# Kernel tuning notes

Hardware: AMD Instinct MI355X
Metric: run time of the kernel (lower is better)

The kernel has to match this reference:

```python
import jax, jax.numpy as jnp
import numpy as np
from jax import lax

EPOCHS = 10  # self.epoch in the torch module


def setup_inputs() -> dict:
    key = jax.random.key(0)
    k1, k2 = jax.random.split(key)
    # (num_patches, groups, channels_per_group, kh, kw)
    patches = jax.random.normal(k1, (40000, 4, 16, 5, 5), dtype=jnp.float32)
    # torch: torch.randn([groups, K, D]) * 0.1
    centroids_init = jax.random.normal(k2, (4, 64, 400), dtype=jnp.float32) * 0.1
    return {"patches": patches, "centroids_init": centroids_init}


def reference(patches, centroids_init):
    N, G, C, H, W = patches.shape
    K = centroids_init.shape[1]
    D = C * H * W
    # [G, N, D] flattened patches per group
    pf = jnp.transpose(patches.reshape(N, G, D), (1, 0, 2))

    def step(centroids, _):
        # half squared norm of each centroid: [G, K]
        c2 = 0.5 * jnp.sum(centroids * centroids, axis=2)
        # scores[g,n,k] = <c_gk, p_gn> - 0.5||c_gk||^2  (max over k == nearest centroid)
        scores = jnp.einsum('gkd,gnd->gnk', centroids, pf) - c2[:, None, :]
        labels = jnp.argmax(scores, axis=2)                       # [G, N]
        S = jax.nn.one_hot(labels, K, dtype=pf.dtype)             # [G, N, K]
        summation = jnp.einsum('gnk,gnd->gkd', S, pf)             # [G, K, D]
        counts = jnp.sum(S, axis=1)                               # [G, K]
        new_c = summation / jnp.where(counts == 0, 1.0, counts)[:, :, None]
        # torch: centroids[:, where(counts==0)[1], :] = 0  -> zero that cluster
        # index across ALL groups if empty in any group
        bad = jnp.any(counts == 0, axis=0)                        # [K]
        new_c = jnp.where(bad[None, :, None], 0.0, new_c)
        return new_c, None

    centroids, _ = lax.scan(step, centroids_init, None, length=EPOCHS)
    # reshape to conv weight layout (out_channels, channels_per_group, kh, kw)
    return centroids.reshape(G * K, C, H, W)
```

## Files before the change

kernel.cpp:

```cpp
#include <hip/hip_runtime.h>

#define NPTS   40000
#define NG     4
#define NK     64
#define ND     400
#define PT     256
#define NCHUNK 25
#define NTILES 157
#define NSPL   16

typedef _Float16 f16x4 __attribute__((ext_vector_type(4)));
typedef float    f32x4 __attribute__((ext_vector_type(4)));

__global__ __launch_bounds__(256)
void assign_kernel(const float* __restrict__ patches,
                   const float* __restrict__ cent,
                   int*   __restrict__ lr,
                   int*   __restrict__ pcnt)
{
    const int g    = blockIdx.y;
    const int tile = blockIdx.x;
    const int t    = threadIdx.x;
    const int n0   = tile * PT;

    __shared__ _Float16 A1[PT][20];
    __shared__ _Float16 A2[PT][20];
    __shared__ _Float16 B1[NK][20];
    __shared__ _Float16 B2[NK][20];
    __shared__ float c2p[NK][4];
    __shared__ float c2s[NK];
    __shared__ int   cnt[NK];

    if (t < NK) cnt[t] = 0;

    {
        int k = t >> 2, j = t & 3;
        const float* c = cent + ((size_t)g * NK + k) * ND + 100 * j;
        float s = 0.0f;
        #pragma unroll
        for (int d = 0; d < 100; d += 4) {
            float4 v = *(const float4*)(c + d);
            s = fmaf(v.x, v.x, fmaf(v.y, v.y, fmaf(v.z, v.z, fmaf(v.w, v.w, s))));
        }
        c2p[k][j] = s;
    }
    __syncthreads();
    if (t < NK) c2s[t] = 2048.0f * (c2p[t][0] + c2p[t][1] + c2p[t][2] + c2p[t][3]);

    const int w   = t >> 6;
    const int l   = t & 63;
    const int q   = l >> 4;
    const int r15 = l & 15;

    int nn = n0 + t; if (nn >= NPTS) nn = NPTS - 1;
    const float* prow = patches + ((size_t)nn * NG + g) * ND;
    const float* crow = cent + ((size_t)g * NK + (t >> 2)) * ND + 4 * (t & 3);

    f32x4 acc[4][4];
    {
        f32x4 z = {0.f, 0.f, 0.f, 0.f};
        #pragma unroll
        for (int i = 0; i < 4; ++i)
            #pragma unroll
            for (int j = 0; j < 4; ++j) acc[i][j] = z;
    }

    float4 pp[4]; float4 pc;
    #pragma unroll
    for (int j = 0; j < 4; ++j) pp[j] = *(const float4*)(prow + 4 * j);
    pc = *(const float4*)(crow);

    for (int c = 0; c < NCHUNK; ++c) {
        #pragma unroll
        for (int j = 0; j < 4; ++j) {
            float4 v = pp[j];
            float s0 = v.x * 64.0f, s1 = v.y * 64.0f, s2 = v.z * 64.0f, s3 = v.w * 64.0f;
            _Float16 a0 = (_Float16)s0, a1 = (_Float16)s1, a2 = (_Float16)s2, a3 = (_Float16)s3;
            f16x4 h1 = {a0, a1, a2, a3};
            f16x4 h2 = {(_Float16)(s0 - (float)a0), (_Float16)(s1 - (float)a1),
                        (_Float16)(s2 - (float)a2), (_Float16)(s3 - (float)a3)};
            *(f16x4*)&A1[t][4 * j] = h1;
            *(f16x4*)&A2[t][4 * j] = h2;
        }
        {
            float4 v = pc;
            float s0 = v.x * 64.0f, s1 = v.y * 64.0f, s2 = v.z * 64.0f, s3 = v.w * 64.0f;
            _Float16 a0 = (_Float16)s0, a1 = (_Float16)s1, a2 = (_Float16)s2, a3 = (_Float16)s3;
            f16x4 h1 = {a0, a1, a2, a3};
            f16x4 h2 = {(_Float16)(s0 - (float)a0), (_Float16)(s1 - (float)a1),
                        (_Float16)(s2 - (float)a2), (_Float16)(s3 - (float)a3)};
            int cc = t >> 2, jj = t & 3;
            *(f16x4*)&B1[cc][4 * jj] = h1;
            *(f16x4*)&B2[cc][4 * jj] = h2;
        }
        __syncthreads();

        if (c + 1 < NCHUNK) {
            const int d0 = (c + 1) * 16;
            #pragma unroll
            for (int j = 0; j < 4; ++j) pp[j] = *(const float4*)(prow + d0 + 4 * j);
            pc = *(const float4*)(crow + d0);
        }

        f16x4 a1v[4], a2v[4], b1v[4], b2v[4];
        #pragma unroll
        for (int pi = 0; pi < 4; ++pi) {
            int p = 64 * w + 16 * pi + r15;
            a1v[pi] = *(const f16x4*)&A1[p][4 * q];
            a2v[pi] = *(const f16x4*)&A2[p][4 * q];
        }
        #pragma unroll
        for (int cj = 0; cj < 4; ++cj) {
            int n = 16 * cj + r15;
            b1v[cj] = *(const f16x4*)&B1[n][4 * q];
            b2v[cj] = *(const f16x4*)&B2[n][4 * q];
        }
        #pragma unroll
        for (int pi = 0; pi < 4; ++pi)
            #pragma unroll
            for (int cj = 0; cj < 4; ++cj) {
                acc[pi][cj] = __builtin_amdgcn_mfma_f32_16x16x16f16(a2v[pi], b1v[cj], acc[pi][cj], 0, 0, 0);
                acc[pi][cj] = __builtin_amdgcn_mfma_f32_16x16x16f16(a1v[pi], b2v[cj], acc[pi][cj], 0, 0, 0);
                acc[pi][cj] = __builtin_amdgcn_mfma_f32_16x16x16f16(a1v[pi], b1v[cj], acc[pi][cj], 0, 0, 0);
            }
        __syncthreads();
    }

    #pragma unroll
    for (int pi = 0; pi < 4; ++pi) {
        #pragma unroll
        for (int r = 0; r < 4; ++r) {
            float m  = acc[pi][0][r] - c2s[r15];
            int best = r15;
            #pragma unroll
            for (int cj = 1; cj < 4; ++cj) {
                int n = 16 * cj + r15;
                float s = acc[pi][cj][r] - c2s[n];
                if (s > m) { m = s; best = n; }
            }
            #pragma unroll
            for (int off = 1; off < 16; off <<= 1) {
                float om = __shfl_xor(m, off);
                int   ob = __shfl_xor(best, off);
                if (om > m || (om == m && ob < best)) { m = om; best = ob; }
            }
            if (r15 == 0) {
                int p  = 64 * w + 16 * pi + 4 * q + r;
                int np = n0 + p;
                if (np < NPTS) {
                    int rk = atomicAdd(&cnt[best], 1);
                    lr[(size_t)g * NPTS + np] = (rk << 8) | best;
                }
            }
        }
    }
    __syncthreads();
    if (t < NK) pcnt[((size_t)g * NTILES + tile) * NK + t] = cnt[t];
}

__global__ __launch_bounds__(256)
void scan_kernel(const int* __restrict__ pcnt,
                 int* __restrict__ tilebase,
                 int* __restrict__ cbase,
                 int* __restrict__ counts)
{
    const int g = blockIdx.x;
    const int t = threadIdx.x;
    __shared__ int cnt_tk[NTILES * NK];
    __shared__ int totals[NK];
    __shared__ int kbase[NK];

    for (int i = t; i < NTILES * NK; i += 256)
        cnt_tk[i] = pcnt[(size_t)g * NTILES * NK + i];
    __syncthreads();

    if (t < NK) {
        int s = 0;
        for (int tl = 0; tl < NTILES; ++tl) s += cnt_tk[tl * NK + t];
        totals[t] = s;
    }
    __syncthreads();
    if (t == 0) {
        int run = 0;
        for (int k = 0; k < NK; ++k) { kbase[k] = run; run += totals[k]; }
    }
    __syncthreads();
    if (t < NK) {
        counts[g * NK + t] = totals[t];
        cbase[g * NK + t]  = kbase[t];
        int run = kbase[t];
        for (int tl = 0; tl < NTILES; ++tl) {
            tilebase[((size_t)g * NTILES + tl) * NK + t] = run;
            run += cnt_tk[tl * NK + t];
        }
    }
}

__global__ __launch_bounds__(256)
void scatter_kernel(const int* __restrict__ lr,
                    const int* __restrict__ tilebase,
                    int* __restrict__ order)
{
    const int tile = blockIdx.x, g = blockIdx.y, t = threadIdx.x;
    const int n = tile * PT + t;
    if (n < NPTS) {
        int packed = lr[(size_t)g * NPTS + n];
        int L = packed & 63, r = packed >> 8;
        order[(size_t)g * NPTS + tilebase[((size_t)g * NTILES + tile) * NK + L] + r] = n;
    }
}

__global__ __launch_bounds__(512, 2)
void gather_kernel(const float* __restrict__ patches,
                   const int*   __restrict__ order,
                   const int*   __restrict__ cbase,
                   const int*   __restrict__ counts,
                   float* __restrict__ psum)
{
    const int s = blockIdx.x, k = blockIdx.y, g = blockIdx.z;
    const int t = threadIdx.x;
    const int base = cbase[g * NK + k];
    const int cnt  = counts[g * NK + k];
    const int start = base + (cnt * s) / NSPL;
    const int end   = base + (cnt * (s + 1)) / NSPL;

    const int slot = t / 100;
    const int q    = t - slot * 100;

    float4 acc = make_float4(0.f, 0.f, 0.f, 0.f);
    if (t < 500) {
        const int* ord = order + (size_t)g * NPTS;
        #pragma unroll 4
        for (int i = start + slot; i < end; i += 5) {
            int n = ord[i];
            float4 v = *(const float4*)(patches + ((size_t)n * NG + g) * ND + 4 * q);
            acc.x += v.x; acc.y += v.y; acc.z += v.z; acc.w += v.w;
        }
    }

    __shared__ float sums[ND];
    for (int i = t; i < ND; i += 512) sums[i] = 0.0f;
    __syncthreads();
    if (t < 500) {
        atomicAdd(&sums[4 * q + 0], acc.x);
        atomicAdd(&sums[4 * q + 1], acc.y);
        atomicAdd(&sums[4 * q + 2], acc.z);
        atomicAdd(&sums[4 * q + 3], acc.w);
    }
    __syncthreads();
    if (t < 100) {
        float* dst = psum + (((size_t)(g * NK + k)) * NSPL + s) * ND + 4 * t;
        *(float4*)dst = *(const float4*)&sums[4 * t];
    }
}

__global__ __launch_bounds__(128)
void update_kernel(const float* __restrict__ psum,
                   const int*   __restrict__ counts,
                   float* __restrict__ outc)
{
    const int gk = blockIdx.x;
    const int g = gk >> 6, k = gk & 63;
    const int t = threadIdx.x;

    const bool bad = (counts[0 * NK + k] == 0) | (counts[1 * NK + k] == 0) |
                     (counts[2 * NK + k] == 0) | (counts[3 * NK + k] == 0);
    const int  c  = counts[g * NK + k];
    const float inv = 1.0f / (float)(c == 0 ? 1 : c);

    if (t < 100) {
        float4 s = make_float4(0.f, 0.f, 0.f, 0.f);
        const float* p = psum + ((size_t)gk * NSPL) * ND + 4 * t;
        #pragma unroll
        for (int sp = 0; sp < NSPL; ++sp) {
            float4 v = *(const float4*)(p + (size_t)sp * ND);
            s.x += v.x; s.y += v.y; s.z += v.z; s.w += v.w;
        }
        float4 o;
        o.x = bad ? 0.0f : s.x * inv;
        o.y = bad ? 0.0f : s.y * inv;
        o.z = bad ? 0.0f : s.z * inv;
        o.w = bad ? 0.0f : s.w * inv;
        *(float4*)(outc + (size_t)gk * ND + 4 * t) = o;
    }
}

extern "C" void kernel_launch(void* const* d_in, const int* in_sizes, int n_in,
                              void* d_out, int out_size, void* d_ws, size_t ws_size,
                              hipStream_t stream)
{
    const float* patches = (const float*)d_in[0];
    const float* cinit   = (const float*)d_in[1];
    float* out = (float*)d_out;

    const size_t CSZ = (size_t)NG * NK * ND;
    float* centA = (float*)d_ws;
    float* centB = centA + CSZ;
    int* lr       = (int*)(centB + CSZ);
    int* pcnt     = lr + (size_t)NG * NPTS;
    int* tilebase = pcnt + (size_t)NG * NTILES * NK;
    int* cbase    = tilebase + (size_t)NG * NTILES * NK;
    int* counts   = cbase + NG * NK;
    int* order    = counts + NG * NK;
    float* psum   = (float*)(order + (size_t)NG * NPTS);

    const float* cur = cinit;
    for (int e = 0; e < 10; ++e) {
        assign_kernel<<<dim3(NTILES, NG), 256, 0, stream>>>(patches, cur, lr, pcnt);
        scan_kernel<<<NG, 256, 0, stream>>>(pcnt, tilebase, cbase, counts);
        scatter_kernel<<<dim3(NTILES, NG), 256, 0, stream>>>(lr, tilebase, order);
        gather_kernel<<<dim3(NSPL, NK, NG), 512, 0, stream>>>(patches, order, cbase, counts, psum);
        float* nxt = (e == 9) ? out : ((e & 1) ? centB : centA);
        update_kernel<<<dim3(NG * NK), 128, 0, stream>>>(psum, counts, nxt);
        cur = nxt;
    }
}
```

Baseline: 1.771 ms.

## Replace counting-sort gather with linear scan and shared-memory atomic accumulation

Removes the scan and scatter kernels and the label-sorted order array. Each block now streams a contiguous range of points, reads them coalesced, and adds each point into a per-cluster accumulator in shared memory using LDS atomics, also counting cluster sizes. The update kernel reduces the 64 per-block partials and rebuilds the counts. This cuts two launches and the random gather per epoch, in exchange for heavy LDS atomic contention, a large shared-memory footprint per block and only 256 blocks in total.

```diff
diff --git a/kernel.cpp b/kernel.cpp
--- a/kernel.cpp
+++ b/kernel.cpp
@@ -7,7 +7,8 @@
 #define PT     256
 #define NCHUNK 25
 #define NTILES 157
-#define NSPL   16
+#define NBLK   64
+#define PPB    625
 
 typedef _Float16 f16x4 __attribute__((ext_vector_type(4)));
 typedef float    f32x4 __attribute__((ext_vector_type(4)));
@@ -15,8 +16,7 @@
 __global__ __launch_bounds__(256)
 void assign_kernel(const float* __restrict__ patches,
                    const float* __restrict__ cent,
-                   int*   __restrict__ lr,
-                   int*   __restrict__ pcnt)
+                   int*   __restrict__ lab)
 {
     const int g    = blockIdx.y;
     const int tile = blockIdx.x;
@@ -29,9 +29,6 @@
     __shared__ _Float16 B2[NK][20];
     __shared__ float c2p[NK][4];
     __shared__ float c2s[NK];
-    __shared__ int   cnt[NK];
-
-    if (t < NK) cnt[t] = 0;
 
     {
         int k = t >> 2, j = t & 3;
@@ -147,133 +144,92 @@
             if (r15 == 0) {
                 int p  = 64 * w + 16 * pi + 4 * q + r;
                 int np = n0 + p;
-                if (np < NPTS) {
-                    int rk = atomicAdd(&cnt[best], 1);
-                    lr[(size_t)g * NPTS + np] = (rk << 8) | best;
-                }
-            }
-        }
-    }
-    __syncthreads();
-    if (t < NK) pcnt[((size_t)g * NTILES + tile) * NK + t] = cnt[t];
-}
-
-__global__ __launch_bounds__(256)
-void scan_kernel(const int* __restrict__ pcnt,
-                 int* __restrict__ tilebase,
-                 int* __restrict__ cbase,
-                 int* __restrict__ counts)
-{
-    const int g = blockIdx.x;
+                if (np < NPTS) lab[(size_t)g * NPTS + np] = best;
+            }
+        }
+    }
+}
+
+__global__ __launch_bounds__(1024)
+void gather_lin(const float* __restrict__ patches,
+                const int*   __restrict__ lab,
+                float* __restrict__ psum,
+                int*   __restrict__ pcnt2)
+{
+    const int b = blockIdx.x, g = blockIdx.y;
     const int t = threadIdx.x;
-    __shared__ int cnt_tk[NTILES * NK];
-    __shared__ int totals[NK];
-    __shared__ int kbase[NK];
-
-    for (int i = t; i < NTILES * NK; i += 256)
-        cnt_tk[i] = pcnt[(size_t)g * NTILES * NK + i];
-    __syncthreads();
-
-    if (t < NK) {
-        int s = 0;
-        for (int tl = 0; tl < NTILES; ++tl) s += cnt_tk[tl * NK + t];
-        totals[t] = s;
-    }
-    __syncthreads();
-    if (t == 0) {
-        int run = 0;
-        for (int k = 0; k < NK; ++k) { kbase[k] = run; run += totals[k]; }
-    }
-    __syncthreads();
-    if (t < NK) {
-        counts[g * NK + t] = totals[t];
-        cbase[g * NK + t]  = kbase[t];
-        int run = kbase[t];
-        for (int tl = 0; tl < NTILES; ++tl) {
-            tilebase[((size_t)g * NTILES + tl) * NK + t] = run;
-            run += cnt_tk[tl * NK + t];
-        }
-    }
-}
-
-__global__ __launch_bounds__(256)
-void scatter_kernel(const int* __restrict__ lr,
-                    const int* __restrict__ tilebase,
-                    int* __restrict__ order)
-{
-    const int tile = blockIdx.x, g = blockIdx.y, t = threadIdx.x;
-    const int n = tile * PT + t;
-    if (n < NPTS) {
-        int packed = lr[(size_t)g * NPTS + n];
-        int L = packed & 63, r = packed >> 8;
-        order[(size_t)g * NPTS + tilebase[((size_t)g * NTILES + tile) * NK + L] + r] = n;
-    }
-}
-
-__global__ __launch_bounds__(512, 2)
-void gather_kernel(const float* __restrict__ patches,
-                   const int*   __restrict__ order,
-                   const int*   __restrict__ cbase,
-                   const int*   __restrict__ counts,
-                   float* __restrict__ psum)
-{
-    const int s = blockIdx.x, k = blockIdx.y, g = blockIdx.z;
-    const int t = threadIdx.x;
-    const int base = cbase[g * NK + k];
-    const int cnt  = counts[g * NK + k];
-    const int start = base + (cnt * s) / NSPL;
-    const int end   = base + (cnt * (s + 1)) / NSPL;
+
+    __shared__ float acc[NK][ND + 4];
+    __shared__ int   cnt[NK];
+
+    for (int i = t; i < NK * (ND + 4); i += 1024) ((float*)acc)[i] = 0.0f;
+    if (t < NK) cnt[t] = 0;
+    __syncthreads();
 
     const int slot = t / 100;
     const int q    = t - slot * 100;
 
-    float4 acc = make_float4(0.f, 0.f, 0.f, 0.f);
-    if (t < 500) {
-        const int* ord = order + (size_t)g * NPTS;
-        #pragma unroll 4
-        for (int i = start + slot; i < end; i += 5) {
-            int n = ord[i];
+    if (t < 1000) {
+        const int* lg = lab + (size_t)g * NPTS;
+        const int start = b * PPB, end = start + PPB;
+        #pragma unroll 2
+        for (int n = start + slot; n < end; n += 10) {
+            int L = lg[n];
             float4 v = *(const float4*)(patches + ((size_t)n * NG + g) * ND + 4 * q);
-            acc.x += v.x; acc.y += v.y; acc.z += v.z; acc.w += v.w;
-        }
-    }
-
-    __shared__ float sums[ND];
-    for (int i = t; i < ND; i += 512) sums[i] = 0.0f;
-    __syncthreads();
-    if (t < 500) {
-        atomicAdd(&sums[4 * q + 0], acc.x);
-        atomicAdd(&sums[4 * q + 1], acc.y);
-        atomicAdd(&sums[4 * q + 2], acc.z);
-        atomicAdd(&sums[4 * q + 3], acc.w);
-    }
-    __syncthreads();
-    if (t < 100) {
-        float* dst = psum + (((size_t)(g * NK + k)) * NSPL + s) * ND + 4 * t;
-        *(float4*)dst = *(const float4*)&sums[4 * t];
-    }
+            atomicAdd(&acc[L][4 * q + 0], v.x);
+            atomicAdd(&acc[L][4 * q + 1], v.y);
+            atomicAdd(&acc[L][4 * q + 2], v.z);
+            atomicAdd(&acc[L][4 * q + 3], v.w);
+            if (q == 0) atomicAdd(&cnt[L], 1);
+        }
+    }
+    __syncthreads();
+
+    float* dst = psum + ((size_t)(g * NBLK + b) * NK) * ND;
+    for (int i = t; i < NK * 100; i += 1024) {
+        int k = i / 100, qq = i - 100 * k;
+        *(float4*)(dst + (size_t)k * ND + 4 * qq) = *(const float4*)&acc[k][4 * qq];
+    }
+    if (t < NK) pcnt2[((size_t)g * NBLK + b) * NK + t] = cnt[t];
 }
 
 __global__ __launch_bounds__(128)
 void update_kernel(const float* __restrict__ psum,
-                   const int*   __restrict__ counts,
+                   const int*   __restrict__ pcnt2,
                    float* __restrict__ outc)
 {
     const int gk = blockIdx.x;
     const int g = gk >> 6, k = gk & 63;
     const int t = threadIdx.x;
 
-    const bool bad = (counts[0 * NK + k] == 0) | (counts[1 * NK + k] == 0) |
-                     (counts[2 * NK + k] == 0) | (counts[3 * NK + k] == 0);
-    const int  c  = counts[g * NK + k];
+    __shared__ int cpart[NG][32];
+    __shared__ int ctot[NG];
+
+    {
+        int gp = t >> 5, bb = t & 31;
+        int s = pcnt2[((size_t)gp * NBLK + bb) * NK + k]
+              + pcnt2[((size_t)gp * NBLK + bb + 32) * NK + k];
+        cpart[gp][bb] = s;
+    }
+    __syncthreads();
+    if (t < NG) {
+        int s = 0;
+        #pragma unroll
+        for (int i = 0; i < 32; ++i) s += cpart[t][i];
+        ctot[t] = s;
+    }
+    __syncthreads();
+
+    const bool bad = (ctot[0] == 0) | (ctot[1] == 0) | (ctot[2] == 0) | (ctot[3] == 0);
+    const int  c   = ctot[g];
     const float inv = 1.0f / (float)(c == 0 ? 1 : c);
 
     if (t < 100) {
         float4 s = make_float4(0.f, 0.f, 0.f, 0.f);
-        const float* p = psum + ((size_t)gk * NSPL) * ND + 4 * t;
-        #pragma unroll
-        for (int sp = 0; sp < NSPL; ++sp) {
-            float4 v = *(const float4*)(p + (size_t)sp * ND);
+        const float* p = psum + (((size_t)g * NBLK) * NK + k) * ND + 4 * t;
+        #pragma unroll 8
+        for (int b = 0; b < NBLK; ++b) {
+            float4 v = *(const float4*)(p + (size_t)b * NK * ND);
             s.x += v.x; s.y += v.y; s.z += v.z; s.w += v.w;
         }
         float4 o;
@@ -281,7 +237,7 @@
         o.y = bad ? 0.0f : s.y * inv;
         o.z = bad ? 0.0f : s.z * inv;
         o.w = bad ? 0.0f : s.w * inv;
-        *(float4*)(outc + (size_t)gk * ND + 4 * t) = o;
+        *(float4*)(outc + (size_t)(g * NK + k) * ND + 4 * t) = o;
     }
 }
 
@@ -296,22 +252,16 @@
     const size_t CSZ = (size_t)NG * NK * ND;
     float* centA = (float*)d_ws;
     float* centB = centA + CSZ;
-    int* lr       = (int*)(centB + CSZ);
-    int* pcnt     = lr + (size_t)NG * NPTS;
-    int* tilebase = pcnt + (size_t)NG * NTILES * NK;
-    int* cbase    = tilebase + (size_t)NG * NTILES * NK;
-    int* counts   = cbase + NG * NK;
-    int* order    = counts + NG * NK;
-    float* psum   = (float*)(order + (size_t)NG * NPTS);
+    int*   lab   = (int*)(centB + CSZ);
+    int*   pcnt2 = lab + (size_t)NG * NPTS;
+    float* psum  = (float*)(pcnt2 + (size_t)NG * NBLK * NK);
 
     const float* cur = cinit;
     for (int e = 0; e < 10; ++e) {
-        assign_kernel<<<dim3(NTILES, NG), 256, 0, stream>>>(patches, cur, lr, pcnt);
-        scan_kernel<<<NG, 256, 0, stream>>>(pcnt, tilebase, cbase, counts);
-        scatter_kernel<<<dim3(NTILES, NG), 256, 0, stream>>>(lr, tilebase, order);
-        gather_kernel<<<dim3(NSPL, NK, NG), 512, 0, stream>>>(patches, order, cbase, counts, psum);
+        assign_kernel<<<dim3(NTILES, NG), 256, 0, stream>>>(patches, cur, lab);
+        gather_lin<<<dim3(NBLK, NG), 1024, 0, stream>>>(patches, lab, psum, pcnt2);
         float* nxt = (e == 9) ? out : ((e & 1) ? centB : centA);
-        update_kernel<<<dim3(NG * NK), 128, 0, stream>>>(psum, counts, nxt);
+        update_kernel<<<dim3(NG * NK), 128, 0, stream>>>(psum, pcnt2, nxt);
         cur = nxt;
     }
 }
```

Result: slower. 4.392 ms (+148.0%).

## Halve assign tile size and fuse scan into scatter kernel

Applied to the files above, without the earlier changes.

Point tiles in the assign kernel shrink from 256 to 128 points. Each thread now loads half a row, and each wave computes 2 MFMA row-blocks instead of 4, which doubles the grid to 313x4 blocks for better CU occupancy. The separate single-block-per-group scan kernel is removed: every scatter block redundantly reduces the per-tile counts in shared memory (as 16-bit values) to get its own prefix and the cluster bases. This saves a launch and a serial stage, at the cost of repeated prefix work per block and double-loading centroid data per tile.

```diff
diff --git a/kernel.cpp b/kernel.cpp
--- a/kernel.cpp
+++ b/kernel.cpp
@@ -4,9 +4,9 @@
 #define NG     4
 #define NK     64
 #define ND     400
-#define PT     256
+#define PT     128
 #define NCHUNK 25
-#define NTILES 157
+#define NTILES 313
 #define NSPL   16
 
 typedef _Float16 f16x4 __attribute__((ext_vector_type(4)));
@@ -52,35 +52,37 @@
     const int q   = l >> 4;
     const int r15 = l & 15;
 
-    int nn = n0 + t; if (nn >= NPTS) nn = NPTS - 1;
-    const float* prow = patches + ((size_t)nn * NG + g) * ND;
+    const int rh = t & 127;
+    const int hh = t >> 7;
+    int nn = n0 + rh; if (nn >= NPTS) nn = NPTS - 1;
+    const float* prow = patches + ((size_t)nn * NG + g) * ND + 8 * hh;
     const float* crow = cent + ((size_t)g * NK + (t >> 2)) * ND + 4 * (t & 3);
 
-    f32x4 acc[4][4];
+    f32x4 acc[2][4];
     {
         f32x4 z = {0.f, 0.f, 0.f, 0.f};
         #pragma unroll
-        for (int i = 0; i < 4; ++i)
+        for (int i = 0; i < 2; ++i)
             #pragma unroll
             for (int j = 0; j < 4; ++j) acc[i][j] = z;
     }
 
-    float4 pp[4]; float4 pc;
-    #pragma unroll
-    for (int j = 0; j < 4; ++j) pp[j] = *(const float4*)(prow + 4 * j);
+    float4 pp[2]; float4 pc;
+    pp[0] = *(const float4*)(prow);
+    pp[1] = *(const float4*)(prow + 4);
     pc = *(const float4*)(crow);
 
     for (int c = 0; c < NCHUNK; ++c) {
         #pragma unroll
-        for (int j = 0; j < 4; ++j) {
-            float4 v = pp[j];
+        for (int j2 = 0; j2 < 2; ++j2) {
+            float4 v = pp[j2];
             float s0 = v.x * 64.0f, s1 = v.y * 64.0f, s2 = v.z * 64.0f, s3 = v.w * 64.0f;
             _Float16 a0 = (_Float16)s0, a1 = (_Float16)s1, a2 = (_Float16)s2, a3 = (_Float16)s3;
             f16x4 h1 = {a0, a1, a2, a3};
             f16x4 h2 = {(_Float16)(s0 - (float)a0), (_Float16)(s1 - (float)a1),
                         (_Float16)(s2 - (float)a2), (_Float16)(s3 - (float)a3)};
-            *(f16x4*)&A1[t][4 * j] = h1;
-            *(f16x4*)&A2[t][4 * j] = h2;
+            *(f16x4*)&A1[rh][8 * hh + 4 * j2] = h1;
+            *(f16x4*)&A2[rh][8 * hh + 4 * j2] = h2;
         }
         {
             float4 v = pc;
@@ -97,15 +99,15 @@
 
         if (c + 1 < NCHUNK) {
             const int d0 = (c + 1) * 16;
-            #pragma unroll
-            for (int j = 0; j < 4; ++j) pp[j] = *(const float4*)(prow + d0 + 4 * j);
+            pp[0] = *(const float4*)(prow + d0);
+            pp[1] = *(const float4*)(prow + d0 + 4);
             pc = *(const float4*)(crow + d0);
         }
 
-        f16x4 a1v[4], a2v[4], b1v[4], b2v[4];
-        #pragma unroll
-        for (int pi = 0; pi < 4; ++pi) {
-            int p = 64 * w + 16 * pi + r15;
+        f16x4 a1v[2], a2v[2], b1v[4], b2v[4];
+        #pragma unroll
+        for (int pi = 0; pi < 2; ++pi) {
+            int p = 32 * w + 16 * pi + r15;
             a1v[pi] = *(const f16x4*)&A1[p][4 * q];
             a2v[pi] = *(const f16x4*)&A2[p][4 * q];
         }
@@ -116,7 +118,7 @@
             b2v[cj] = *(const f16x4*)&B2[n][4 * q];
         }
         #pragma unroll
-        for (int pi = 0; pi < 4; ++pi)
+        for (int pi = 0; pi < 2; ++pi)
             #pragma unroll
             for (int cj = 0; cj < 4; ++cj) {
                 acc[pi][cj] = __builtin_amdgcn_mfma_f32_16x16x16f16(a2v[pi], b1v[cj], acc[pi][cj], 0, 0, 0);
@@ -127,7 +129,7 @@
     }
 
     #pragma unroll
-    for (int pi = 0; pi < 4; ++pi) {
+    for (int pi = 0; pi < 2; ++pi) {
         #pragma unroll
         for (int r = 0; r < 4; ++r) {
             float m  = acc[pi][0][r] - c2s[r15];
@@ -145,7 +147,7 @@
                 if (om > m || (om == m && ob < best)) { m = om; best = ob; }
             }
             if (r15 == 0) {
-                int p  = 64 * w + 16 * pi + 4 * q + r;
+                int p  = 32 * w + 16 * pi + 4 * q + r;
                 int np = n0 + p;
                 if (np < NPTS) {
                     int rk = atomicAdd(&cnt[best], 1);
@@ -159,54 +161,55 @@
 }
 
 __global__ __launch_bounds__(256)
-void scan_kernel(const int* __restrict__ pcnt,
-                 int* __restrict__ tilebase,
-                 int* __restrict__ cbase,
-                 int* __restrict__ counts)
-{
-    const int g = blockIdx.x;
-    const int t = threadIdx.x;
-    __shared__ int cnt_tk[NTILES * NK];
-    __shared__ int totals[NK];
+void scatter2_kernel(const int* __restrict__ lr,
+                     const int* __restrict__ pcnt,
+                     int* __restrict__ order,
+                     int* __restrict__ cbase,
+                     int* __restrict__ counts)
+{
+    const int tile = blockIdx.x, g = blockIdx.y, t = threadIdx.x;
+    __shared__ unsigned short cnt_tk[NTILES * NK];
+    __shared__ int part [4][NK];
+    __shared__ int part2[4][NK];
     __shared__ int kbase[NK];
-
+    __shared__ int tpre[NK];
+
+    const int* pg = pcnt + (size_t)g * NTILES * NK;
     for (int i = t; i < NTILES * NK; i += 256)
-        cnt_tk[i] = pcnt[(size_t)g * NTILES * NK + i];
-    __syncthreads();
-
+        cnt_tk[i] = (unsigned short)pg[i];
+    __syncthreads();
+
+    {
+        int k = t & 63, p = t >> 6;
+        int s1 = 0, s2 = 0;
+        for (int tl = p; tl < NTILES; tl += 4) {
+            int v = cnt_tk[tl * NK + k];
+            s1 += v;
+            if (tl < tile) s2 += v;
+        }
+        part [p][k] = s1;
+        part2[p][k] = s2;
+    }
+    __syncthreads();
     if (t < NK) {
-        int s = 0;
-        for (int tl = 0; tl < NTILES; ++tl) s += cnt_tk[tl * NK + t];
-        totals[t] = s;
+        part[0][t] = part[0][t] + part[1][t] + part[2][t] + part[3][t];
+        tpre[t]    = part2[0][t] + part2[1][t] + part2[2][t] + part2[3][t];
     }
     __syncthreads();
     if (t == 0) {
         int run = 0;
-        for (int k = 0; k < NK; ++k) { kbase[k] = run; run += totals[k]; }
-    }
-    __syncthreads();
-    if (t < NK) {
-        counts[g * NK + t] = totals[t];
+        for (int k = 0; k < NK; ++k) { kbase[k] = run; run += part[0][k]; }
+    }
+    __syncthreads();
+    if (tile == 0 && t < NK) {
         cbase[g * NK + t]  = kbase[t];
-        int run = kbase[t];
-        for (int tl = 0; tl < NTILES; ++tl) {
-            tilebase[((size_t)g * NTILES + tl) * NK + t] = run;
-            run += cnt_tk[tl * NK + t];
-        }
-    }
-}
-
-__global__ __launch_bounds__(256)
-void scatter_kernel(const int* __restrict__ lr,
-                    const int* __restrict__ tilebase,
-                    int* __restrict__ order)
-{
-    const int tile = blockIdx.x, g = blockIdx.y, t = threadIdx.x;
+        counts[g * NK + t] = part[0][t];
+    }
     const int n = tile * PT + t;
-    if (n < NPTS) {
+    if (t < PT && n < NPTS) {
         int packed = lr[(size_t)g * NPTS + n];
         int L = packed & 63, r = packed >> 8;
-        order[(size_t)g * NPTS + tilebase[((size_t)g * NTILES + tile) * NK + L] + r] = n;
+        order[(size_t)g * NPTS + kbase[L] + tpre[L] + r] = n;
     }
 }
 
@@ -298,8 +301,7 @@
     float* centB = centA + CSZ;
     int* lr       = (int*)(centB + CSZ);
     int* pcnt     = lr + (size_t)NG * NPTS;
-    int* tilebase = pcnt + (size_t)NG * NTILES * NK;
-    int* cbase    = tilebase + (size_t)NG * NTILES * NK;
+    int* cbase    = pcnt + (size_t)NG * NTILES * NK;
     int* counts   = cbase + NG * NK;
     int* order    = counts + NG * NK;
     float* psum   = (float*)(order + (size_t)NG * NPTS);
@@ -307,8 +309,7 @@
     const float* cur = cinit;
     for (int e = 0; e < 10; ++e) {
         assign_kernel<<<dim3(NTILES, NG), 256, 0, stream>>>(patches, cur, lr, pcnt);
-        scan_kernel<<<NG, 256, 0, stream>>>(pcnt, tilebase, cbase, counts);
-        scatter_kernel<<<dim3(NTILES, NG), 256, 0, stream>>>(lr, tilebase, order);
+        scatter2_kernel<<<dim3(NTILES, NG), 256, 0, stream>>>(lr, pcnt, order, cbase, counts);
         gather_kernel<<<dim3(NSPL, NK, NG), 512, 0, stream>>>(patches, order, cbase, counts, psum);
         float* nxt = (e == 9) ? out : ((e & 1) ? centB : centA);
         update_kernel<<<dim3(NG * NK), 128, 0, stream>>>(psum, counts, nxt);
```

Result: faster. 1.723 ms (-2.7%).
